# Kernel tuning notes

Hardware: AMD Instinct MI355X
Metric: run time of the kernel (lower is better)

The kernel has to match this reference:

```python
import jax, jax.numpy as jnp
import numpy as np

LOSS_WEIGHT = 1.0
TAL = 0.07
N_USE = 100  # foreground=False path uses first 100 boxes


def setup_inputs() -> dict:
    key = jax.random.key(0)
    k1, k2, k3 = jax.random.split(key, 3)
    d, s_n, n_box = 512, 150000, 4096
    attribute_vec = jax.random.normal(k1, (d, s_n), dtype=jnp.float32)
    feature = jax.random.normal(k2, (n_box, d), dtype=jnp.float32)
    label = jax.random.randint(k3, (n_box,), 0, s_n, dtype=jnp.int64)
    return {"attribute_vec": attribute_vec, "feature": feature, "label": label}


def reference(attribute_vec, feature, label):
    # foreground=False: take first 100 boxes
    fea = feature[:N_USE]            # [n, d]
    lab = label[:N_USE]              # [n]
    n = N_USE
    # cosine-similarity logits scaled by 1/tal: [s_n, n]
    value_all = jnp.einsum('ds,nd->sn', attribute_vec, fea)
    fea_norm = jnp.linalg.norm(fea, axis=1)            # [n]
    att_norm = jnp.linalg.norm(attribute_vec, axis=0)  # [s_n]
    ex_all = value_all / (TAL * att_norm[:, None] * fea_norm[None, :])
    # per-sample loss: -log( exp(pos) / sum_s exp(ex) ) == -log_softmax over class axis at label
    logp = jax.nn.log_softmax(ex_all, axis=0)          # [s_n, n]
    pos_logp = logp[lab, jnp.arange(n)]                # [n]
    loss = -jnp.sum(pos_logp)
    return LOSS_WEIGHT * loss / n
```

## Files before the change

### kernel.cpp

```cpp
#include <hip/hip_runtime.h>
#include <hip/hip_bf16.h>

#define S_N   150000
#define DIM   512
#define NUSE  100
#define NPAD  112
#define TALF  0.07f
#define BS    128
#define NBLK  ((S_N + BS - 1) / BS)
#define NCHUNK (DIM / 32)

using short8 = __attribute__((ext_vector_type(8))) short;
using f32x4  = __attribute__((ext_vector_type(4))) float;

__device__ __forceinline__ short f2bf(float f) {
    union { float f; unsigned u; } x; x.f = f;
    unsigned r = x.u + 0x7FFF + ((x.u >> 16) & 1);
    return (short)(r >> 16);
}

__global__ void prep_b(const float* __restrict__ fea, short8* __restrict__ Bws,
                       float* __restrict__ gsum) {
    int idx = blockIdx.x * 256 + threadIdx.x;
    if (blockIdx.x == 0 && threadIdx.x < NPAD) gsum[threadIdx.x] = 0.f;
    int c    = idx / 448;
    int r    = idx % 448;
    int tn   = r / 64;
    int lane = r % 64;
    int n     = tn * 16 + (lane & 15);
    int dbase = c * 32 + ((lane >> 4) & 3) * 8;
    const float* fp = fea + n * DIM + dbase;
    short8 o;
#pragma unroll
    for (int j = 0; j < 8; ++j) o[j] = f2bf(fp[j]);
    Bws[idx] = o;
}

__global__ void prep_norm_pos(const float* __restrict__ attr, const float* __restrict__ fea,
                              const int* __restrict__ label,
                              float* __restrict__ invf_tal, float* __restrict__ expos) {
    int wv   = blockIdx.x * 4 + (threadIdx.x >> 6);
    int lane = threadIdx.x & 63;
    if (wv >= NPAD) return;
    const float* f = fea + wv * DIM;
    float ss = 0.f;
#pragma unroll
    for (int j = 0; j < 8; ++j) { float v = f[lane * 8 + j]; ss += v * v; }
    for (int o = 1; o < 64; o <<= 1) ss += __shfl_xor(ss, o);
    if (lane == 0) invf_tal[wv] = rsqrtf(ss) * (1.0f / TALF);
    if (wv < NUSE) {
        int lab = label[wv];
        float dt = 0.f, aq = 0.f;
#pragma unroll
        for (int j = 0; j < 8; ++j) {
            int d = j * 64 + lane;
            float a  = attr[(size_t)d * S_N + lab];
            float fe = f[d];
            dt += a * fe; aq += a * a;
        }
        for (int o = 1; o < 64; o <<= 1) { dt += __shfl_xor(dt, o); aq += __shfl_xor(aq, o); }
        if (lane == 0) expos[wv] = dt * rsqrtf(aq) * rsqrtf(ss) * (1.0f / TALF);
    }
}

__global__ __launch_bounds__(256, 3)
void main_gemm(const float* __restrict__ A, const short8* __restrict__ Bws,
               const float* __restrict__ invf_tal, float* __restrict__ gsum) {
    __shared__ float psum[4][NPAD];
    const int tid  = threadIdx.x;
    const int w    = tid >> 6, lane = tid & 63;
    const int q    = lane >> 4, l16 = lane & 15;
    const int s0   = blockIdx.x * BS;
    const int srow0 = s0 + w * 32 + l16;
    const bool v0 = srow0 < S_N;
    const bool v1 = srow0 + 16 < S_N;

    const float* a0 = A + (size_t)(q * 8) * S_N + srow0;

    f32x4 acc[2][7];
#pragma unroll
    for (int mt = 0; mt < 2; ++mt)
#pragma unroll
        for (int tn = 0; tn < 7; ++tn) acc[mt][tn] = f32x4{0.f, 0.f, 0.f, 0.f};

    float ss0 = 0.f, ss1 = 0.f;
    float raw0[8], raw1[8];
#pragma unroll
    for (int j = 0; j < 8; ++j) {
        raw0[j] = v0 ? a0[(size_t)j * S_N] : 0.f;
        raw1[j] = v1 ? a0[(size_t)j * S_N + 16] : 0.f;
    }
    const short8* bp = Bws + lane;

    for (int c = 0; c < NCHUNK; ++c) {
        short8 bfr[7];
#pragma unroll
        for (int tn = 0; tn < 7; ++tn) bfr[tn] = bp[(c * 7 + tn) * 64];
        short8 af0, af1;
#pragma unroll
        for (int j = 0; j < 8; ++j) {
            float x0 = raw0[j], x1 = raw1[j];
            ss0 += x0 * x0; ss1 += x1 * x1;
            af0[j] = f2bf(x0); af1[j] = f2bf(x1);
        }
        if (c + 1 < NCHUNK) {
            const float* an = a0 + (size_t)(c + 1) * 32 * S_N;
#pragma unroll
            for (int j = 0; j < 8; ++j) {
                raw0[j] = v0 ? an[(size_t)j * S_N] : 0.f;
                raw1[j] = v1 ? an[(size_t)j * S_N + 16] : 0.f;
            }
        }
#pragma unroll
        for (int tn = 0; tn < 7; ++tn) {
            acc[0][tn] = __builtin_amdgcn_mfma_f32_16x16x32_bf16(af0, bfr[tn], acc[0][tn], 0, 0, 0);
            acc[1][tn] = __builtin_amdgcn_mfma_f32_16x16x32_bf16(af1, bfr[tn], acc[1][tn], 0, 0, 0);
        }
    }

    ss0 += __shfl_xor(ss0, 16); ss0 += __shfl_xor(ss0, 32);
    ss1 += __shfl_xor(ss1, 16); ss1 += __shfl_xor(ss1, 32);
    float inva0 = v0 ? rsqrtf(ss0) : 0.f;
    float inva1 = v1 ? rsqrtf(ss1) : 0.f;
    float ir0[4], ir1[4];
#pragma unroll
    for (int reg = 0; reg < 4; ++reg) {
        ir0[reg] = __shfl(inva0, q * 4 + reg);
        ir1[reg] = __shfl(inva1, q * 4 + reg);
    }
    float invf_l[7];
#pragma unroll
    for (int tn = 0; tn < 7; ++tn) invf_l[tn] = invf_tal[tn * 16 + l16];

    const float M = 1.0f / TALF;
    const int rowbase = s0 + w * 32 + q * 4;
#pragma unroll
    for (int tn = 0; tn < 7; ++tn) {
        float sacc = 0.f;
#pragma unroll
        for (int reg = 0; reg < 4; ++reg) {
            bool rv0 = (rowbase + reg) < S_N;
            bool rv1 = (rowbase + 16 + reg) < S_N;
            float ex0 = acc[0][tn][reg] * ir0[reg] * invf_l[tn];
            float ex1 = acc[1][tn][reg] * ir1[reg] * invf_l[tn];
            sacc += rv0 ? __expf(ex0 - M) : 0.f;
            sacc += rv1 ? __expf(ex1 - M) : 0.f;
        }
        sacc += __shfl_xor(sacc, 16);
        sacc += __shfl_xor(sacc, 32);
        if (lane < 16) psum[w][tn * 16 + lane] = sacc;
    }
    __syncthreads();
    if (tid < NPAD) {
        float t = psum[0][tid] + psum[1][tid] + psum[2][tid] + psum[3][tid];
        atomicAdd(&gsum[tid], t);
    }
}

__global__ void finalize(const float* __restrict__ gsum, const float* __restrict__ expos,
                         float* __restrict__ out) {
    __shared__ float r[128];
    int tid = threadIdx.x;
    const float M = 1.0f / TALF;
    float v = 0.f;
    if (tid < NUSE) v = (M + logf(gsum[tid])) - expos[tid];
    r[tid] = v;
    __syncthreads();
    for (int s = 64; s > 0; s >>= 1) {
        if (tid < s) r[tid] += r[tid + s];
        __syncthreads();
    }
    if (tid == 0) out[0] = r[0] * (1.0f / NUSE);
}

extern "C" void kernel_launch(void* const* d_in, const int* in_sizes, int n_in,
                              void* d_out, int out_size, void* d_ws, size_t ws_size,
                              hipStream_t stream) {
    const float* attr  = (const float*)d_in[0];
    const float* fea   = (const float*)d_in[1];
    const int*   label = (const int*)d_in[2];
    float* out = (float*)d_out;

    char* ws = (char*)d_ws;
    short8* Bws      = (short8*)ws;
    float* invf_tal  = (float*)(ws + 114688);
    float* expos     = (float*)(ws + 115136);
    float* gsum      = (float*)(ws + 115584);

    prep_b<<<28, 256, 0, stream>>>(fea, Bws, gsum);
    prep_norm_pos<<<28, 256, 0, stream>>>(attr, fea, label, invf_tal, expos);
    main_gemm<<<NBLK, 256, 0, stream>>>(attr, Bws, invf_tal, gsum);
    finalize<<<1, 128, 0, stream>>>(gsum, expos, out);
}
```

Before: 435.5 us.

## Stage A tiles through LDS with async global_load_lds double buffering

Replaces per-thread strided register loads of the attribute matrix with direct global-to-LDS 16-byte async loads into a double-buffered shared tile, then reads fragments from LDS. The tail block is shifted back to overlap the previous block, and the overlapping rows are masked out, so bounds checks on loads disappear. This aims for wider, coalesced 16-byte global transactions and overlap of the next chunk's fetch with MFMA work. In exchange it adds a block barrier per chunk and 32KB of LDS, which may reduce occupancy, and LDS reads may hit bank conflicts.

```diff
diff --git a/kernel.cpp b/kernel.cpp
--- a/kernel.cpp
+++ b/kernel.cpp
@@ -1,5 +1,6 @@
 #include <hip/hip_runtime.h>
 #include <hip/hip_bf16.h>
+#include <stdint.h>
 
 #define S_N   150000
 #define DIM   512
@@ -63,19 +64,30 @@
     }
 }
 
+__device__ __forceinline__ void gl2lds16(const float* gptr, char* lptr) {
+    __builtin_amdgcn_global_load_lds(
+        (const __attribute__((address_space(1))) unsigned*)(uintptr_t)gptr,
+        (__attribute__((address_space(3))) unsigned*)(uintptr_t)lptr,
+        16, 0, 0);
+}
+
 __global__ __launch_bounds__(256, 3)
 void main_gemm(const float* __restrict__ A, const short8* __restrict__ Bws,
                const float* __restrict__ invf_tal, float* __restrict__ gsum) {
+    __shared__ float buf[2][32][BS];
     __shared__ float psum[4][NPAD];
+
     const int tid  = threadIdx.x;
     const int w    = tid >> 6, lane = tid & 63;
     const int q    = lane >> 4, l16 = lane & 15;
-    const int s0   = blockIdx.x * BS;
-    const int srow0 = s0 + w * 32 + l16;
-    const bool v0 = srow0 < S_N;
-    const bool v1 = srow0 + 16 < S_N;
-
-    const float* a0 = A + (size_t)(q * 8) * S_N + srow0;
+
+    const bool tail = (blockIdx.x == NBLK - 1);
+    const int s_base = tail ? (S_N - BS) : blockIdx.x * BS;
+    const int minr   = tail ? ((NBLK - 1) * BS - (S_N - BS)) : 0;
+
+    const float* gsrc = A + (size_t)(tid >> 5) * S_N + s_base + (tid & 31) * 4;
+    char* lds_w0 = (char*)&buf[0][0][0] + w * 1024;
+    char* lds_w1 = (char*)&buf[1][0][0] + w * 1024;
 
     f32x4 acc[2][7];
 #pragma unroll
@@ -84,32 +96,34 @@
         for (int tn = 0; tn < 7; ++tn) acc[mt][tn] = f32x4{0.f, 0.f, 0.f, 0.f};
 
     float ss0 = 0.f, ss1 = 0.f;
-    float raw0[8], raw1[8];
-#pragma unroll
-    for (int j = 0; j < 8; ++j) {
-        raw0[j] = v0 ? a0[(size_t)j * S_N] : 0.f;
-        raw1[j] = v1 ? a0[(size_t)j * S_N + 16] : 0.f;
-    }
     const short8* bp = Bws + lane;
 
+#pragma unroll
+    for (int i = 0; i < 4; ++i)
+        gl2lds16(gsrc + (size_t)i * 8 * S_N, lds_w0 + i * 4096);
+
     for (int c = 0; c < NCHUNK; ++c) {
+        const int pc = c & 1;
+        __syncthreads();
+        if (c + 1 < NCHUNK) {
+            const float* gn = gsrc + (size_t)(c + 1) * 32 * S_N;
+            char* ldsn = ((c + 1) & 1) ? lds_w1 : lds_w0;
+#pragma unroll
+            for (int i = 0; i < 4; ++i)
+                gl2lds16(gn + (size_t)i * 8 * S_N, ldsn + i * 4096);
+        }
+
         short8 bfr[7];
 #pragma unroll
         for (int tn = 0; tn < 7; ++tn) bfr[tn] = bp[(c * 7 + tn) * 64];
+
         short8 af0, af1;
 #pragma unroll
         for (int j = 0; j < 8; ++j) {
-            float x0 = raw0[j], x1 = raw1[j];
+            float x0 = buf[pc][q * 8 + j][w * 32 + l16];
+            float x1 = buf[pc][q * 8 + j][w * 32 + l16 + 16];
             ss0 += x0 * x0; ss1 += x1 * x1;
             af0[j] = f2bf(x0); af1[j] = f2bf(x1);
-        }
-        if (c + 1 < NCHUNK) {
-            const float* an = a0 + (size_t)(c + 1) * 32 * S_N;
-#pragma unroll
-            for (int j = 0; j < 8; ++j) {
-                raw0[j] = v0 ? an[(size_t)j * S_N] : 0.f;
-                raw1[j] = v1 ? an[(size_t)j * S_N + 16] : 0.f;
-            }
         }
 #pragma unroll
         for (int tn = 0; tn < 7; ++tn) {
@@ -120,8 +134,8 @@
 
     ss0 += __shfl_xor(ss0, 16); ss0 += __shfl_xor(ss0, 32);
     ss1 += __shfl_xor(ss1, 16); ss1 += __shfl_xor(ss1, 32);
-    float inva0 = v0 ? rsqrtf(ss0) : 0.f;
-    float inva1 = v1 ? rsqrtf(ss1) : 0.f;
+    float inva0 = rsqrtf(ss0);
+    float inva1 = rsqrtf(ss1);
     float ir0[4], ir1[4];
 #pragma unroll
     for (int reg = 0; reg < 4; ++reg) {
@@ -133,14 +147,14 @@
     for (int tn = 0; tn < 7; ++tn) invf_l[tn] = invf_tal[tn * 16 + l16];
 
     const float M = 1.0f / TALF;
-    const int rowbase = s0 + w * 32 + q * 4;
+    const int rloc = w * 32 + q * 4;
 #pragma unroll
     for (int tn = 0; tn < 7; ++tn) {
         float sacc = 0.f;
 #pragma unroll
         for (int reg = 0; reg < 4; ++reg) {
-            bool rv0 = (rowbase + reg) < S_N;
-            bool rv1 = (rowbase + 16 + reg) < S_N;
+            bool rv0 = (rloc + reg) >= minr;
+            bool rv1 = (rloc + 16 + reg) >= minr;
             float ex0 = acc[0][tn][reg] * ir0[reg] * invf_l[tn];
             float ex1 = acc[1][tn][reg] * ir1[reg] * invf_l[tn];
             sacc += rv0 ? __expf(ex0 - M) : 0.f;
```

After: 437.4 us. About the same (+0.4%).
